# Kernel tuning notes

Hardware: AMD Instinct MI355X
Metric: run time of the kernel (lower is better)

The kernel has to match this reference:

```python
import jax, jax.numpy as jnp
import numpy as np

B, T, IN, H = 64, 256, 512, 1024


def setup_inputs() -> dict:
    key = jax.random.key(0)
    ks = jax.random.split(key, 21)
    stdv = 1.0 / float(np.sqrt(H))
    u = lambda k, shape: jax.random.uniform(k, shape, jnp.float32, -stdv, stdv)
    inp = {"input": jax.random.normal(ks[0], (B, T, IN), jnp.float32)}
    idx = 1
    for g in ("f", "i", "o", "c"):
        inp[f"W_{g}"] = u(ks[idx], (H, IN)); idx += 1
        inp[f"W_{g}_mask"] = u(ks[idx], (H, IN)); idx += 1
        inp[f"U_{g}"] = u(ks[idx], (H, H)); idx += 1
        inp[f"U_{g}_mask"] = u(ks[idx], (H, H)); idx += 1
        inp[f"b_{g}"] = u(ks[idx], (H,)); idx += 1
    return inp


def reference(input, W_f, W_f_mask, U_f, U_f_mask, b_f,
              W_i, W_i_mask, U_i, U_i_mask, b_i,
              W_o, W_o_mask, U_o, U_o_mask, b_o,
              W_c, W_c_mask, U_c, U_c_mask, b_c):
    # MaskedParameterMatrix with wise='feat': sigmoid(x @ W_mask^T) * (x @ W^T)
    def ml(x, W, Wm):
        return jax.nn.sigmoid(x @ Wm.T) * (x @ W.T)

    def step(carry, x_t):  # x_t: [B, IN]
        h, c = carry  # each [B, H]
        f = jax.nn.sigmoid(ml(x_t, W_f, W_f_mask) + ml(h, U_f, U_f_mask) + b_f)
        # NOTE: original module computes the input gate but never uses it (bug kept for fidelity)
        i = jax.nn.sigmoid(ml(x_t, W_i, W_i_mask) + ml(h, U_i, U_i_mask) + b_i)
        o = jax.nn.sigmoid(ml(x_t, W_o, W_o_mask) + ml(h, U_o, U_o_mask) + b_o)
        c = f * c + jnp.tanh(ml(x_t, W_c, W_c_mask) + ml(h, U_c, U_c_mask) + b_c)
        h = o * c
        return (h, c), h

    b, hdim = input.shape[0], W_f.shape[0]
    h0 = jnp.zeros((b, hdim), input.dtype)
    (hT, cT), ys = jax.lax.scan(step, (h0, h0), jnp.swapaxes(input, 0, 1))
    output = jnp.swapaxes(ys, 0, 1)  # [B, T, H]
    # final states shaped [1, B, H] as in the torch module (after transpose)
    return output, (hT[None], cT[None])
```

## Files before the change

kernel.cpp:

```cpp
#include <hip/hip_runtime.h>
#include <hip/hip_bf16.h>


typedef __attribute__((ext_vector_type(8))) short bfrag;
typedef __attribute__((ext_vector_type(4))) float f32x4;

__device__ __forceinline__ unsigned short f2b(float v) {
  __hip_bfloat16 h = __float2bfloat16(v);
  union { __hip_bfloat16 h; unsigned short u; } c; c.h = h; return c.u;
}
__device__ __forceinline__ float b2f(unsigned short u) {
  union { unsigned int i; float f; } c; c.i = ((unsigned int)u) << 16; return c.f;
}
__device__ __forceinline__ float sigm(float x) { return 1.0f / (1.0f + __expf(-x)); }
__device__ __forceinline__ float tanh_f(float x) {
  float e = __expf(2.0f * x);
  return (e - 1.0f) / (e + 1.0f);
}

__global__ __launch_bounds__(512, 2) void xproj_kernel(
    const float* __restrict__ inp,
    const float* __restrict__ Wf, const float* __restrict__ Wmf,
    const float* __restrict__ Wo, const float* __restrict__ Wmo,
    const float* __restrict__ Wc, const float* __restrict__ Wmc,
    unsigned short* __restrict__ mlx)
{
  __shared__ unsigned short Al[256 * 128];
  __shared__ unsigned short Bl[256 * 128];

  const int tid = threadIdx.x;
  const int w = tid >> 6, l = tid & 63;
  const int c = l & 15, g4 = l >> 4;
  const int jc = blockIdx.x, gate = blockIdx.y, tq = blockIdx.z;
  const float* W  = (gate == 0) ? Wf  : (gate == 1) ? Wo  : Wc;
  const float* Wm = (gate == 0) ? Wmf : (gate == 1) ? Wmo : Wmc;
  const int j0 = jc * 128;

  f32x4 acc[2][16];
#pragma unroll
  for (int mi = 0; mi < 2; ++mi)
#pragma unroll
    for (int ni = 0; ni < 16; ++ni) acc[mi][ni] = (f32x4){0.f, 0.f, 0.f, 0.f};

  for (int kc = 0; kc < 4; ++kc) {
#pragma unroll
    for (int i = 0; i < 16; ++i) {
      int idx = tid + i * 512;
      int row = idx >> 5;
      int xl  = idx & 31;
      int b_ = row & 63, tl = row >> 6;
      const float4 va = *(const float4*)(inp + (size_t)(b_ * 256 + tq * 4 + tl) * 512 + kc * 128 + xl * 4);
      ushort4 pa;
      pa.x = f2b(va.x); pa.y = f2b(va.y); pa.z = f2b(va.z); pa.w = f2b(va.w);
      *(ushort4*)((char*)Al + ((row * 256 + xl * 8) ^ ((row & 7) << 4))) = pa;
      const float* src = (row < 128) ? (W + (size_t)(j0 + row) * 512)
                                     : (Wm + (size_t)(j0 + row - 128) * 512);
      const float4 vb = *(const float4*)(src + kc * 128 + xl * 4);
      ushort4 pb;
      pb.x = f2b(vb.x); pb.y = f2b(vb.y); pb.z = f2b(vb.z); pb.w = f2b(vb.w);
      *(ushort4*)((char*)Bl + ((row * 256 + xl * 8) ^ ((row & 7) << 4))) = pb;
    }
    __syncthreads();
#pragma unroll
    for (int ks = 0; ks < 4; ++ks) {
      const int koff = (ks * 32 + g4 * 8) * 2;
      bfrag af[2];
#pragma unroll
      for (int mi = 0; mi < 2; ++mi) {
        int row = w * 32 + mi * 16 + c;
        af[mi] = *(const bfrag*)((const char*)Al + ((row * 256 + koff) ^ ((row & 7) << 4)));
      }
#pragma unroll
      for (int ni = 0; ni < 16; ++ni) {
        int n = ni * 16 + c;
        bfrag bf = *(const bfrag*)((const char*)Bl + ((n * 256 + koff) ^ ((n & 7) << 4)));
#pragma unroll
        for (int mi = 0; mi < 2; ++mi)
          acc[mi][ni] = __builtin_amdgcn_mfma_f32_16x16x32_bf16(af[mi], bf, acc[mi][ni], 0, 0, 0);
      }
    }
    __syncthreads();
  }
#pragma unroll
  for (int mi = 0; mi < 2; ++mi) {
#pragma unroll
    for (int ni = 0; ni < 8; ++ni) {
      f32x4 xw = acc[mi][ni];
      f32x4 xm = acc[mi][ni + 8];
      ushort4 st;
      st.x = f2b(xw[0] * sigm(xm[0]));
      st.y = f2b(xw[1] * sigm(xm[1]));
      st.z = f2b(xw[2] * sigm(xm[2]));
      st.w = f2b(xw[3] * sigm(xm[3]));
      int row = w * 32 + mi * 16 + g4 * 4;
      int tl = row >> 6, b_ = row & 63;
      int j = j0 + ni * 16 + c;
      size_t addr = ((size_t)((tq * 4 + tl) * 3 + gate) * 1024 + j) * 64 + b_;
      *(ushort4*)(mlx + addr) = st;
    }
  }
}

__global__ __launch_bounds__(256, 1) void recur_kernel(
    const float* __restrict__ Uf, const float* __restrict__ Umf,
    const float* __restrict__ Uo, const float* __restrict__ Umo,
    const float* __restrict__ Uc, const float* __restrict__ Umc,
    const float* __restrict__ bfp, const float* __restrict__ bop,
    const float* __restrict__ bcp,
    const unsigned short* __restrict__ mlx,
    unsigned short* __restrict__ hx,
    float* __restrict__ cfin,
    unsigned int* __restrict__ flg)
{
  __shared__ float prep[4 * 48 * 68];

  __builtin_amdgcn_fence(__ATOMIC_ACQUIRE, "agent");

  const int tid = threadIdx.x;
  const int bid = blockIdx.x;
  const int w = tid >> 6, l = tid & 63;
  const int c = l & 15, g4 = l >> 4;
  const int j0 = bid * 8;

  bfrag Breg[3][8];
#pragma unroll
  for (int nt = 0; nt < 3; ++nt) {
    const int n = nt * 16 + c;
    const int mi6 = n >> 3;
    const float* src = (mi6 == 0) ? Uf : (mi6 == 1) ? Umf : (mi6 == 2) ? Uo
                     : (mi6 == 3) ? Umo : (mi6 == 4) ? Uc : Umc;
    src += (size_t)(j0 + (n & 7)) * 1024;
#pragma unroll
    for (int ks = 0; ks < 8; ++ks) {
      const int k = w * 256 + ks * 32 + g4 * 8;
      const float4 v0 = *(const float4*)(src + k);
      const float4 v1 = *(const float4*)(src + k + 4);
      bfrag b;
      b[0] = (short)f2b(v0.x); b[1] = (short)f2b(v0.y);
      b[2] = (short)f2b(v0.z); b[3] = (short)f2b(v0.w);
      b[4] = (short)f2b(v1.x); b[5] = (short)f2b(v1.y);
      b[6] = (short)f2b(v1.z); b[7] = (short)f2b(v1.w);
      Breg[nt][ks] = b;
    }
  }

  const int jh = tid >> 6;
  const int bb = tid & 63;
  const int cl0 = jh * 2;
  float bias[2][3], cr[2] = {0.f, 0.f};
  float mf[2], mo[2], mc[2];
#pragma unroll
  for (int q = 0; q < 2; ++q) {
    bias[q][0] = bfp[j0 + cl0 + q];
    bias[q][1] = bop[j0 + cl0 + q];
    bias[q][2] = bcp[j0 + cl0 + q];
  }
  {
    size_t mb = (size_t)(j0 + cl0) * 64 + bb;
#pragma unroll
    for (int q = 0; q < 2; ++q) {
      mf[q] = b2f(mlx[mb + q * 64]);
      mo[q] = b2f(mlx[mb + 65536 + q * 64]);
      mc[q] = b2f(mlx[mb + 2 * 65536 + q * 64]);
    }
  }

  for (int t = 0; t < 256; ++t) {
    if (t > 0) {
      const unsigned int* fp = flg + (size_t)t * 128 + w * 32 + l;
      unsigned int v = 1;
      while (true) {
        if (l < 32) v = __hip_atomic_load(fp, __ATOMIC_RELAXED, __HIP_MEMORY_SCOPE_AGENT);
        if (__all(v != 0)) break;
        __builtin_amdgcn_s_sleep(1);
      }
      asm volatile("" ::: "memory");
    }
    const unsigned short* hr = hx + (size_t)t * 65536;

    f32x4 acc[4][3];
#pragma unroll
    for (int mi = 0; mi < 4; ++mi)
#pragma unroll
      for (int nt = 0; nt < 3; ++nt) acc[mi][nt] = (f32x4){0.f, 0.f, 0.f, 0.f};

#pragma unroll
    for (int ks = 0; ks < 8; ++ks) {
      const int k = w * 256 + ks * 32 + g4 * 8;
#pragma unroll
      for (int mi = 0; mi < 4; ++mi) {
        const bfrag af = *(const bfrag*)(hr + (size_t)(mi * 16 + c) * 1024 + k);
#pragma unroll
        for (int nt = 0; nt < 3; ++nt)
          acc[mi][nt] = __builtin_amdgcn_mfma_f32_16x16x32_bf16(af, Breg[nt][ks], acc[mi][nt], 0, 0, 0);
      }
    }
#pragma unroll
    for (int mi = 0; mi < 4; ++mi)
#pragma unroll
      for (int nt = 0; nt < 3; ++nt) {
        int col = nt * 16 + c;
        *(f32x4*)&prep[(w * 48 + col) * 68 + mi * 16 + g4 * 4] = acc[mi][nt];
      }
    __syncthreads();

    unsigned int pack = 0;
#pragma unroll
    for (int q = 0; q < 2; ++q) {
      const int cl = cl0 + q;
      float s[6];
#pragma unroll
      for (int m = 0; m < 6; ++m) {
        const int col = m * 8 + cl;
        s[m] = prep[col * 68 + bb] + prep[(48 + col) * 68 + bb] +
               prep[(96 + col) * 68 + bb] + prep[(144 + col) * 68 + bb];
      }
      float fg = sigm(mf[q] + sigm(s[1]) * s[0] + bias[q][0]);
      float og = sigm(mo[q] + sigm(s[3]) * s[2] + bias[q][1]);
      float cd = tanh_f(mc[q] + sigm(s[5]) * s[4] + bias[q][2]);
      cr[q] = fg * cr[q] + cd;
      float hv = og * cr[q];
      pack |= (unsigned int)f2b(hv) << (16 * q);
      if (t == 255) cfin[(size_t)(j0 + cl) * 64 + bb] = cr[q];
    }
    __hip_atomic_store((unsigned int*)(hx + (size_t)(t + 1) * 65536 + (size_t)bb * 1024 + j0 + cl0),
                       pack, __ATOMIC_RELAXED, __HIP_MEMORY_SCOPE_AGENT);
    __syncthreads();

    if (tid == 0)
      __hip_atomic_store(&flg[(size_t)(t + 1) * 128 + bid], 1u,
                         __ATOMIC_RELAXED, __HIP_MEMORY_SCOPE_AGENT);

    if (t < 255) {
      size_t mb = (size_t)(t + 1) * 3 * 65536 + (size_t)(j0 + cl0) * 64 + bb;
#pragma unroll
      for (int q = 0; q < 2; ++q) {
        mf[q] = b2f(mlx[mb + q * 64]);
        mo[q] = b2f(mlx[mb + 65536 + q * 64]);
        mc[q] = b2f(mlx[mb + 2 * 65536 + q * 64]);
      }
    }
  }
}

__global__ __launch_bounds__(256) void histcast_kernel(
    const unsigned short* __restrict__ hx, float* __restrict__ out)
{
  const int b = blockIdx.x >> 8, t = blockIdx.x & 255;
  const unsigned short* src = hx + ((size_t)(t + 1) * 64 + b) * 1024;
  float* dst = out + ((size_t)b * 256 + t) * 1024;
  const int j = threadIdx.x * 4;
  ushort4 v = *(const ushort4*)(src + j);
  float4 o;
  o.x = b2f(v.x); o.y = b2f(v.y); o.z = b2f(v.z); o.w = b2f(v.w);
  *(float4*)(dst + j) = o;
}

__global__ __launch_bounds__(256) void finals_kernel(
    const unsigned short* __restrict__ hx, const float* __restrict__ cfin,
    float* __restrict__ out)
{
  int tid = blockIdx.x * 256 + threadIdx.x;
  int b = tid >> 10, j = tid & 1023;
  out[16777216 + tid]         = b2f(hx[(size_t)256 * 65536 + (size_t)b * 1024 + j]);
  out[16777216 + 65536 + tid] = cfin[(size_t)j * 64 + b];
}

extern "C" void kernel_launch(void* const* d_in, const int* in_sizes, int n_in,
                              void* d_out, int out_size, void* d_ws, size_t ws_size,
                              hipStream_t stream)
{
  const float* input = (const float*)d_in[0];
  const float* W_f  = (const float*)d_in[1];
  const float* Wm_f = (const float*)d_in[2];
  const float* U_f  = (const float*)d_in[3];
  const float* Um_f = (const float*)d_in[4];
  const float* b_f  = (const float*)d_in[5];
  const float* W_o  = (const float*)d_in[11];
  const float* Wm_o = (const float*)d_in[12];
  const float* U_o  = (const float*)d_in[13];
  const float* Um_o = (const float*)d_in[14];
  const float* b_o  = (const float*)d_in[15];
  const float* W_c  = (const float*)d_in[16];
  const float* Wm_c = (const float*)d_in[17];
  const float* U_c  = (const float*)d_in[18];
  const float* Um_c = (const float*)d_in[19];
  const float* b_c  = (const float*)d_in[20];

  char* ws = (char*)d_ws;
  size_t off = 0;
  unsigned short* mlx = (unsigned short*)(ws + off); off += (size_t)256 * 3 * 1024 * 64 * 2;
  unsigned short* hx  = (unsigned short*)(ws + off); off += (size_t)257 * 64 * 1024 * 2;
  float* cfin = (float*)(ws + off);                  off += (size_t)1024 * 64 * 4;
  unsigned int* flg = (unsigned int*)(ws + off);     off += (size_t)257 * 128 * 4;
  if (off > ws_size) return;

  hipMemsetAsync(hx, 0, 131072, stream);
  hipMemsetAsync(flg, 0, (size_t)257 * 128 * 4, stream);

  xproj_kernel<<<dim3(8, 3, 64), 512, 0, stream>>>(input, W_f, Wm_f, W_o, Wm_o, W_c, Wm_c, mlx);
  recur_kernel<<<128, 256, 0, stream>>>(U_f, Um_f, U_o, Um_o, U_c, Um_c,
                                        b_f, b_o, b_c, mlx, hx, cfin, flg);
  histcast_kernel<<<16384, 256, 0, stream>>>(hx, (float*)d_out);
  finals_kernel<<<256, 256, 0, stream>>>(hx, cfin, (float*)d_out);
}
```

Measured before the change: 2.341 ms.

## Use per-wave arrival flags, blocked h layout, and double-buffered LDS in recurrence

Replaces the per-block flag with per-wave flags written right after each wave's h store. Waiters poll 64-bit flag pairs without sleeping, and the second __syncthreads per timestep is removed by double-buffering the LDS reduction buffer. The hidden-state history moves to a blocked [t][k/8][b][8] layout so each MFMA A-fragment load and each h store are contiguous. The histcast and finals kernels are adapted to the new layout. In exchange it adds more flag traffic and busy spinning, and relies on relaxed stores plus vmcnt waits for ordering.

```diff
diff --git a/kernel.cpp b/kernel.cpp
--- a/kernel.cpp
+++ b/kernel.cpp
@@ -110,9 +110,9 @@
     const unsigned short* __restrict__ mlx,
     unsigned short* __restrict__ hx,
     float* __restrict__ cfin,
-    unsigned int* __restrict__ flg)
-{
-  __shared__ float prep[4 * 48 * 68];
+    unsigned int* __restrict__ sent)
+{
+  __shared__ float prep[2][4 * 48 * 68];
 
   __builtin_amdgcn_fence(__ATOMIC_ACQUIRE, "agent");
 
@@ -144,9 +144,8 @@
     }
   }
 
-  const int jh = tid >> 6;
-  const int bb = tid & 63;
-  const int cl0 = jh * 2;
+  const int bb = l;
+  const int cl0 = w * 2;
   float bias[2][3], cr[2] = {0.f, 0.f};
   float mf[2], mo[2], mc[2];
 #pragma unroll
@@ -167,16 +166,15 @@
 
   for (int t = 0; t < 256; ++t) {
     if (t > 0) {
-      const unsigned int* fp = flg + (size_t)t * 128 + w * 32 + l;
-      unsigned int v = 1;
+      const unsigned long long* sp =
+          (const unsigned long long*)(sent + (size_t)t * 512 + w * 128 + 2 * l);
       while (true) {
-        if (l < 32) v = __hip_atomic_load(fp, __ATOMIC_RELAXED, __HIP_MEMORY_SCOPE_AGENT);
-        if (__all(v != 0)) break;
-        __builtin_amdgcn_s_sleep(1);
-      }
+        unsigned long long v = __hip_atomic_load(sp, __ATOMIC_RELAXED, __HIP_MEMORY_SCOPE_AGENT);
+        if (__all(v == 0x0000000100000001ULL)) break;
+      }
+      __builtin_amdgcn_sched_barrier(0);
       asm volatile("" ::: "memory");
     }
-    const unsigned short* hr = hx + (size_t)t * 65536;
 
     f32x4 acc[4][3];
 #pragma unroll
@@ -186,21 +184,22 @@
 
 #pragma unroll
     for (int ks = 0; ks < 8; ++ks) {
-      const int k = w * 256 + ks * 32 + g4 * 8;
+      const int kb = w * 32 + ks * 4 + g4;
 #pragma unroll
       for (int mi = 0; mi < 4; ++mi) {
-        const bfrag af = *(const bfrag*)(hr + (size_t)(mi * 16 + c) * 1024 + k);
+        const bfrag af = *(const bfrag*)(hx + (((size_t)t * 128 + kb) * 64 + mi * 16 + c) * 8);
 #pragma unroll
         for (int nt = 0; nt < 3; ++nt)
           acc[mi][nt] = __builtin_amdgcn_mfma_f32_16x16x32_bf16(af, Breg[nt][ks], acc[mi][nt], 0, 0, 0);
       }
     }
+    float* pp = prep[t & 1];
 #pragma unroll
     for (int mi = 0; mi < 4; ++mi)
 #pragma unroll
       for (int nt = 0; nt < 3; ++nt) {
         int col = nt * 16 + c;
-        *(f32x4*)&prep[(w * 48 + col) * 68 + mi * 16 + g4 * 4] = acc[mi][nt];
+        *(f32x4*)&pp[(w * 48 + col) * 68 + mi * 16 + g4 * 4] = acc[mi][nt];
       }
     __syncthreads();
 
@@ -212,8 +211,8 @@
 #pragma unroll
       for (int m = 0; m < 6; ++m) {
         const int col = m * 8 + cl;
-        s[m] = prep[col * 68 + bb] + prep[(48 + col) * 68 + bb] +
-               prep[(96 + col) * 68 + bb] + prep[(144 + col) * 68 + bb];
+        s[m] = pp[col * 68 + bb] + pp[(48 + col) * 68 + bb] +
+               pp[(96 + col) * 68 + bb] + pp[(144 + col) * 68 + bb];
       }
       float fg = sigm(mf[q] + sigm(s[1]) * s[0] + bias[q][0]);
       float og = sigm(mo[q] + sigm(s[3]) * s[2] + bias[q][1]);
@@ -223,12 +222,13 @@
       pack |= (unsigned int)f2b(hv) << (16 * q);
       if (t == 255) cfin[(size_t)(j0 + cl) * 64 + bb] = cr[q];
     }
-    __hip_atomic_store((unsigned int*)(hx + (size_t)(t + 1) * 65536 + (size_t)bb * 1024 + j0 + cl0),
-                       pack, __ATOMIC_RELAXED, __HIP_MEMORY_SCOPE_AGENT);
-    __syncthreads();
-
-    if (tid == 0)
-      __hip_atomic_store(&flg[(size_t)(t + 1) * 128 + bid], 1u,
+    __hip_atomic_store(
+        (unsigned int*)(hx + ((((size_t)(t + 1) * 128 + bid) * 64 + bb) * 8 + cl0)),
+        pack, __ATOMIC_RELAXED, __HIP_MEMORY_SCOPE_AGENT);
+
+    asm volatile("s_waitcnt vmcnt(0)" ::: "memory");
+    if (l == 0)
+      __hip_atomic_store(&sent[(size_t)(t + 1) * 512 + bid * 4 + w], 1u,
                          __ATOMIC_RELAXED, __HIP_MEMORY_SCOPE_AGENT);
 
     if (t < 255) {
@@ -243,17 +243,20 @@
   }
 }
 
-__global__ __launch_bounds__(256) void histcast_kernel(
+__global__ __launch_bounds__(128) void histcast_kernel(
     const unsigned short* __restrict__ hx, float* __restrict__ out)
 {
   const int b = blockIdx.x >> 8, t = blockIdx.x & 255;
-  const unsigned short* src = hx + ((size_t)(t + 1) * 64 + b) * 1024;
-  float* dst = out + ((size_t)b * 256 + t) * 1024;
-  const int j = threadIdx.x * 4;
-  ushort4 v = *(const ushort4*)(src + j);
-  float4 o;
-  o.x = b2f(v.x); o.y = b2f(v.y); o.z = b2f(v.z); o.w = b2f(v.w);
-  *(float4*)(dst + j) = o;
+  const int j = threadIdx.x * 8;
+  const unsigned short* src = hx + (((size_t)(t + 1) * 128 + (j >> 3)) * 64 + b) * 8;
+  float* dst = out + ((size_t)b * 256 + t) * 1024 + j;
+  ushort4 v0 = *(const ushort4*)(src);
+  ushort4 v1 = *(const ushort4*)(src + 4);
+  float4 o0, o1;
+  o0.x = b2f(v0.x); o0.y = b2f(v0.y); o0.z = b2f(v0.z); o0.w = b2f(v0.w);
+  o1.x = b2f(v1.x); o1.y = b2f(v1.y); o1.z = b2f(v1.z); o1.w = b2f(v1.w);
+  *(float4*)(dst) = o0;
+  *(float4*)(dst + 4) = o1;
 }
 
 __global__ __launch_bounds__(256) void finals_kernel(
@@ -262,7 +265,7 @@
 {
   int tid = blockIdx.x * 256 + threadIdx.x;
   int b = tid >> 10, j = tid & 1023;
-  out[16777216 + tid]         = b2f(hx[(size_t)256 * 65536 + (size_t)b * 1024 + j]);
+  out[16777216 + tid]         = b2f(hx[(((size_t)256 * 128 + (j >> 3)) * 64 + b) * 8 + (j & 7)]);
   out[16777216 + 65536 + tid] = cfin[(size_t)j * 64 + b];
 }
 
@@ -290,17 +293,17 @@
   char* ws = (char*)d_ws;
   size_t off = 0;
   unsigned short* mlx = (unsigned short*)(ws + off); off += (size_t)256 * 3 * 1024 * 64 * 2;
-  unsigned short* hx  = (unsigned short*)(ws + off); off += (size_t)257 * 64 * 1024 * 2;
+  unsigned short* hx  = (unsigned short*)(ws + off); off += (size_t)257 * 128 * 64 * 8 * 2;
   float* cfin = (float*)(ws + off);                  off += (size_t)1024 * 64 * 4;
-  unsigned int* flg = (unsigned int*)(ws + off);     off += (size_t)257 * 128 * 4;
+  unsigned int* sent = (unsigned int*)(ws + off);    off += (size_t)257 * 512 * 4;
   if (off > ws_size) return;
 
   hipMemsetAsync(hx, 0, 131072, stream);
-  hipMemsetAsync(flg, 0, (size_t)257 * 128 * 4, stream);
+  hipMemsetAsync(sent, 0, (size_t)257 * 512 * 4, stream);
 
   xproj_kernel<<<dim3(8, 3, 64), 512, 0, stream>>>(input, W_f, Wm_f, W_o, Wm_o, W_c, Wm_c, mlx);
   recur_kernel<<<128, 256, 0, stream>>>(U_f, Um_f, U_o, Um_o, U_c, Um_c,
-                                        b_f, b_o, b_c, mlx, hx, cfin, flg);
-  histcast_kernel<<<16384, 256, 0, stream>>>(hx, (float*)d_out);
+                                        b_f, b_o, b_c, mlx, hx, cfin, sent);
+  histcast_kernel<<<16384, 128, 0, stream>>>(hx, (float*)d_out);
   finals_kernel<<<256, 256, 0, stream>>>(hx, cfin, (float*)d_out);
 }
```

After: 2.271 ms. -3.0%, faster.
